# Performance work log

Hardware: AMD Instinct MI355X
Metric: run time of the kernel (lower is better)

Reference implementation:

```python
import jax, jax.numpy as jnp
import numpy as np
from jax import lax

M, T, WINDOW = 4096, 2048, 25
NEG_DIAG = -1e10  # matches alphas.fill_diagonal_(-1e10)


def setup_inputs() -> dict:
    key = jax.random.key(0)
    k_ys, k_a, k_r, k_b0, k_b1 = jax.random.split(key, 5)
    ys = jax.random.uniform(k_ys, (M, T), dtype=jnp.float32) * 10.0  # case counts
    alphas = 0.01 * jax.random.normal(k_a, (M, M), dtype=jnp.float32)
    repro = 1.0 + 0.01 * jax.random.normal(k_r, (M, WINDOW), dtype=jnp.float32)  # init ones
    b0 = 0.1 * jax.random.normal(k_b0, (M, 1), dtype=jnp.float32)
    b1 = 0.01 * jax.random.normal(k_b1, (M, 1), dtype=jnp.float32)
    t = jnp.arange(T, dtype=jnp.int32) + 1
    return {"ys": ys, "alphas": alphas, "repro": repro, "b0": b0, "b1": b1, "t": t}


def reference(ys, alphas, repro, b0, b1, t):
    m, _ = ys.shape
    window = repro.shape[1]
    offset = window - 1
    # metapopulation weights: sigmoid adjacency with diagonal forced to ~0
    diag = jnp.eye(m, dtype=bool)
    W = jax.nn.sigmoid(jnp.where(diag, jnp.asarray(NEG_DIAG, ys.dtype), alphas))
    # depthwise conv1d (cross-correlation), groups=M, VALID padding -> (M, T-window+1)
    Z = lax.conv_general_dilated(
        ys[None],                 # (1, M, T)
        repro[:, None, :],        # (M, 1, window)
        window_strides=(1,),
        padding='VALID',
        feature_group_count=m,
        dimension_numbers=('NCH', 'OIH', 'NCH'),
    )[0]                          # (M, T')
    ys_n = ys[:, offset:]         # (M, T')
    # beta_net: per-node softplus-linear in time -> (M, T), then narrow
    tt = t.astype(ys.dtype)
    beta = jax.nn.softplus(b0 + b1 * tt[None, :])[:, offset:]  # (M, T')
    return beta * (jax.nn.softplus(Z) + W @ ys_n)
```

## Files before the change

### kernel.cpp

```cpp
#include <hip/hip_runtime.h>
#include <stdint.h>

#define M_DIM 4096
#define T_DIM 2048
#define N_OUT 2024
#define N_PAD 2048
#define WIN   25
#define K_DIM 4096

typedef short bf16x8 __attribute__((ext_vector_type(8)));
typedef float f32x4  __attribute__((ext_vector_type(4)));

__device__ __forceinline__ unsigned short f2bf(float x) {
  unsigned u = __float_as_uint(x);
  u += 0x7FFF + ((u >> 16) & 1);
  return (unsigned short)(u >> 16);
}
__device__ __forceinline__ float bf2f(unsigned short h) {
  return __uint_as_float(((unsigned)h) << 16);
}

__device__ __forceinline__ void gl2lds16(const void* g, void* l) {
  __builtin_amdgcn_global_load_lds(
      (const __attribute__((address_space(1))) unsigned int*)g,
      (__attribute__((address_space(3))) unsigned int*)l, 16, 0, 0);
}

__global__ __launch_bounds__(256) void k_wcast(const float* __restrict__ alphas,
                                               unsigned short* __restrict__ Wb) {
  size_t i4 = ((size_t)blockIdx.x * 256 + threadIdx.x) * 4;
  const float4 v = *(const float4*)(alphas + i4);
  int row = (int)(i4 >> 12);
  int col = (int)(i4 & 4095);
  float a[4] = {v.x, v.y, v.z, v.w};
  ushort4 o;
  unsigned short* op = (unsigned short*)&o;
#pragma unroll
  for (int j = 0; j < 4; ++j) {
    float w = (row == col + j) ? 0.f : 1.f / (1.f + __expf(-a[j]));
    op[j] = f2bf(w);
  }
  *(ushort4*)(Wb + i4) = o;
}

__global__ __launch_bounds__(256) void k_conv(const float* __restrict__ ys,
                                              const float* __restrict__ repro,
                                              unsigned short* __restrict__ Sbf) {
  __shared__ float sy[256 + WIN - 1];
  __shared__ float sr[WIN];
  int m = blockIdx.y;
  int j0 = blockIdx.x * 256;
  int tid = threadIdx.x;
  sy[tid] = ys[(size_t)m * T_DIM + j0 + tid];
  if (tid < WIN - 1) {
    int jj = j0 + 256 + tid;
    sy[256 + tid] = (jj < T_DIM) ? ys[(size_t)m * T_DIM + jj] : 0.f;
  }
  if (tid < WIN) sr[tid] = repro[m * WIN + tid];
  __syncthreads();
  int j = j0 + tid;
  float z = 0.f;
#pragma unroll
  for (int k = 0; k < WIN; ++k) z += sy[tid + k] * sr[k];
  float sp = fmaxf(z, 0.f) + log1pf(__expf(-fabsf(z)));
  Sbf[(size_t)m * N_PAD + j] = (j < N_OUT) ? f2bf(sp) : (unsigned short)0;
}

__global__ __launch_bounds__(256) void k_transpose(const float* __restrict__ ys,
                                                   unsigned short* __restrict__ BT) {
  __shared__ float t[32][33];
  int n0 = blockIdx.x * 32;
  int k0 = blockIdx.y * 32;
  int tx = threadIdx.x;
  int ty = threadIdx.y;
#pragma unroll
  for (int r = 0; r < 4; ++r) {
    int kk = k0 + ty + r * 8;
    int n = n0 + tx;
    t[ty + r * 8][tx] = (n < N_OUT) ? ys[(size_t)kk * T_DIM + n + (WIN - 1)] : 0.f;
  }
  __syncthreads();
#pragma unroll
  for (int r = 0; r < 4; ++r) {
    int n = n0 + ty + r * 8;
    int kk = k0 + tx;
    BT[(size_t)n * K_DIM + kk] = f2bf(t[tx][ty + r * 8]);
  }
}

__global__ __launch_bounds__(256) void k_gemm(const unsigned short* __restrict__ Wb,
                                              const unsigned short* __restrict__ BT,
                                              const unsigned short* __restrict__ Sbf,
                                              const float* __restrict__ b0,
                                              const float* __restrict__ b1,
                                              float* __restrict__ out) {
  __shared__ __align__(16) unsigned short lA[128 * 32];
  __shared__ __align__(16) unsigned short lB[128 * 32];
  const int tid  = threadIdx.x;
  const int wave = tid >> 6;
  const int lane = tid & 63;
  const int wm = wave >> 1, wn = wave & 1;
  const int m16  = lane & 15;
  const int quad = lane >> 4;
  const int kof  = quad * 8;
  const int tileM = blockIdx.y * 128;
  const int tileN = blockIdx.x * 128;

  f32x4 acc[4][4];
#pragma unroll
  for (int i = 0; i < 4; ++i)
#pragma unroll
    for (int j = 0; j < 4; ++j) acc[i][j] = f32x4{0.f, 0.f, 0.f, 0.f};

  for (int kt = 0; kt < K_DIM / 32; ++kt) {
    const int k0 = kt * 32;
#pragma unroll
    for (int c = 0; c < 2; ++c) {
      int f = c * 256 + tid;
      int row = f >> 2;
      int colb = (f & 3) << 4;
      const char* gA = (const char*)Wb + (((size_t)(tileM + row) * K_DIM + k0) << 1) + colb;
      const char* gB = (const char*)BT + (((size_t)(tileN + row) * K_DIM + k0) << 1) + colb;
      gl2lds16(gA, (char*)lA + c * 4096 + wave * 1024);
      gl2lds16(gB, (char*)lB + c * 4096 + wave * 1024);
    }
    __syncthreads();
    bf16x8 aF[4], bF[4];
#pragma unroll
    for (int i = 0; i < 4; ++i) {
      aF[i] = *(const bf16x8*)&lA[(wm * 64 + i * 16 + m16) * 32 + kof];
      bF[i] = *(const bf16x8*)&lB[(wn * 64 + i * 16 + m16) * 32 + kof];
    }
#pragma unroll
    for (int i = 0; i < 4; ++i)
#pragma unroll
      for (int j = 0; j < 4; ++j)
        acc[i][j] = __builtin_amdgcn_mfma_f32_16x16x32_bf16(aF[i], bF[j], acc[i][j], 0, 0, 0);
    __syncthreads();
  }

#pragma unroll
  for (int j = 0; j < 4; ++j) {
    int gn = tileN + wn * 64 + j * 16 + m16;
    if (gn >= N_OUT) continue;
    float tval = (float)(gn + WIN);
#pragma unroll
    for (int i = 0; i < 4; ++i) {
#pragma unroll
      for (int r = 0; r < 4; ++r) {
        int gm = tileM + wm * 64 + i * 16 + quad * 4 + r;
        float x = b0[gm] + b1[gm] * tval;
        float beta = fmaxf(x, 0.f) + log1pf(__expf(-fabsf(x)));
        float s = bf2f(Sbf[(size_t)gm * N_PAD + gn]);
        out[(size_t)gm * N_OUT + gn] = beta * (s + acc[i][j][r]);
      }
    }
  }
}

extern "C" void kernel_launch(void* const* d_in, const int* in_sizes, int n_in,
                              void* d_out, int out_size, void* d_ws, size_t ws_size,
                              hipStream_t stream) {
  const float* ys     = (const float*)d_in[0];
  const float* alphas = (const float*)d_in[1];
  const float* repro  = (const float*)d_in[2];
  const float* b0     = (const float*)d_in[3];
  const float* b1     = (const float*)d_in[4];
  float* out = (float*)d_out;

  char* ws = (char*)d_ws;
  unsigned short* Wb  = (unsigned short*)ws;
  unsigned short* BT  = (unsigned short*)(ws + (size_t)M_DIM * K_DIM * 2);
  unsigned short* Sbf = (unsigned short*)(ws + (size_t)M_DIM * K_DIM * 2
                                             + (size_t)N_PAD * K_DIM * 2);

  k_wcast<<<(M_DIM * (size_t)K_DIM) / 4 / 256, 256, 0, stream>>>(alphas, Wb);
  k_conv<<<dim3(T_DIM / 256, M_DIM), 256, 0, stream>>>(ys, repro, Sbf);
  k_transpose<<<dim3(N_PAD / 32, K_DIM / 32), dim3(32, 8), 0, stream>>>(ys, BT);
  k_gemm<<<dim3(N_PAD / 128, M_DIM / 128), 256, 0, stream>>>(Wb, BT, Sbf, b0, b1, out);
}
```

Measured before the change: 295.3 us.

## Use 8 waves per GEMM block and widen sigmoid-cast stores

The GEMM block grows from 4 to 8 waves arranged 2x4, so each wave computes a 64x32 sub-tile with half as many accumulators. Each thread now issues one global-to-LDS load per operand per k-step, and the base pointers are hoisted out of the loop. This is meant to raise wave-level parallelism and hide memory latency, at the cost of more LDS fragment reads per MFMA and more barrier participants. Separately, the weight-cast kernel processes 8 elements per thread with 16-byte stores.

```diff
diff --git a/kernel.cpp b/kernel.cpp
--- a/kernel.cpp
+++ b/kernel.cpp
@@ -28,19 +28,20 @@
 
 __global__ __launch_bounds__(256) void k_wcast(const float* __restrict__ alphas,
                                                unsigned short* __restrict__ Wb) {
-  size_t i4 = ((size_t)blockIdx.x * 256 + threadIdx.x) * 4;
-  const float4 v = *(const float4*)(alphas + i4);
-  int row = (int)(i4 >> 12);
-  int col = (int)(i4 & 4095);
-  float a[4] = {v.x, v.y, v.z, v.w};
-  ushort4 o;
-  unsigned short* op = (unsigned short*)&o;
+  size_t i8 = ((size_t)blockIdx.x * 256 + threadIdx.x) * 8;
+  const float4 v0 = *(const float4*)(alphas + i8);
+  const float4 v1 = *(const float4*)(alphas + i8 + 4);
+  int row = (int)(i8 >> 12);
+  int col = (int)(i8 & 4095);
+  float a[8] = {v0.x, v0.y, v0.z, v0.w, v1.x, v1.y, v1.z, v1.w};
+  ushort4 o[2];
+  unsigned short* op = (unsigned short*)o;
 #pragma unroll
-  for (int j = 0; j < 4; ++j) {
+  for (int j = 0; j < 8; ++j) {
     float w = (row == col + j) ? 0.f : 1.f / (1.f + __expf(-a[j]));
     op[j] = f2bf(w);
   }
-  *(ushort4*)(Wb + i4) = o;
+  *(uint4*)(Wb + i8) = *(uint4*)o;
 }
 
 __global__ __launch_bounds__(256) void k_conv(const float* __restrict__ ys,
@@ -88,60 +89,60 @@
   }
 }
 
-__global__ __launch_bounds__(256) void k_gemm(const unsigned short* __restrict__ Wb,
-                                              const unsigned short* __restrict__ BT,
-                                              const unsigned short* __restrict__ Sbf,
-                                              const float* __restrict__ b0,
-                                              const float* __restrict__ b1,
-                                              float* __restrict__ out) {
+__global__ __launch_bounds__(512, 4) void k_gemm(const unsigned short* __restrict__ Wb,
+                                                 const unsigned short* __restrict__ BT,
+                                                 const unsigned short* __restrict__ Sbf,
+                                                 const float* __restrict__ b0,
+                                                 const float* __restrict__ b1,
+                                                 float* __restrict__ out) {
   __shared__ __align__(16) unsigned short lA[128 * 32];
   __shared__ __align__(16) unsigned short lB[128 * 32];
   const int tid  = threadIdx.x;
   const int wave = tid >> 6;
   const int lane = tid & 63;
-  const int wm = wave >> 1, wn = wave & 1;
+  const int wm = wave >> 2;
+  const int wn = wave & 3;
   const int m16  = lane & 15;
   const int quad = lane >> 4;
   const int kof  = quad * 8;
   const int tileM = blockIdx.y * 128;
   const int tileN = blockIdx.x * 128;
 
-  f32x4 acc[4][4];
+  const int srow  = tid >> 2;
+  const int scolb = (tid & 3) << 4;
+
+  f32x4 acc[4][2];
 #pragma unroll
   for (int i = 0; i < 4; ++i)
 #pragma unroll
-    for (int j = 0; j < 4; ++j) acc[i][j] = f32x4{0.f, 0.f, 0.f, 0.f};
+    for (int j = 0; j < 2; ++j) acc[i][j] = f32x4{0.f, 0.f, 0.f, 0.f};
+
+  const char* gA0 = (const char*)Wb + (((size_t)(tileM + srow) * K_DIM) << 1) + scolb;
+  const char* gB0 = (const char*)BT + (((size_t)(tileN + srow) * K_DIM) << 1) + scolb;
 
   for (int kt = 0; kt < K_DIM / 32; ++kt) {
-    const int k0 = kt * 32;
+    const size_t kb = (size_t)kt * 64;
+    gl2lds16(gA0 + kb, (char*)lA + wave * 1024);
+    gl2lds16(gB0 + kb, (char*)lB + wave * 1024);
+    __syncthreads();
+    bf16x8 aF[4], bF[2];
 #pragma unroll
-    for (int c = 0; c < 2; ++c) {
-      int f = c * 256 + tid;
-      int row = f >> 2;
-      int colb = (f & 3) << 4;
-      const char* gA = (const char*)Wb + (((size_t)(tileM + row) * K_DIM + k0) << 1) + colb;
-      const char* gB = (const char*)BT + (((size_t)(tileN + row) * K_DIM + k0) << 1) + colb;
-      gl2lds16(gA, (char*)lA + c * 4096 + wave * 1024);
-      gl2lds16(gB, (char*)lB + c * 4096 + wave * 1024);
-    }
-    __syncthreads();
-    bf16x8 aF[4], bF[4];
+    for (int i = 0; i < 4; ++i)
+      aF[i] = *(const bf16x8*)&lA[(wm * 64 + i * 16 + m16) * 32 + kof];
 #pragma unroll
-    for (int i = 0; i < 4; ++i) {
-      aF[i] = *(const bf16x8*)&lA[(wm * 64 + i * 16 + m16) * 32 + kof];
-      bF[i] = *(const bf16x8*)&lB[(wn * 64 + i * 16 + m16) * 32 + kof];
-    }
+    for (int j = 0; j < 2; ++j)
+      bF[j] = *(const bf16x8*)&lB[(wn * 32 + j * 16 + m16) * 32 + kof];
 #pragma unroll
     for (int i = 0; i < 4; ++i)
 #pragma unroll
-      for (int j = 0; j < 4; ++j)
+      for (int j = 0; j < 2; ++j)
         acc[i][j] = __builtin_amdgcn_mfma_f32_16x16x32_bf16(aF[i], bF[j], acc[i][j], 0, 0, 0);
     __syncthreads();
   }
 
 #pragma unroll
-  for (int j = 0; j < 4; ++j) {
-    int gn = tileN + wn * 64 + j * 16 + m16;
+  for (int j = 0; j < 2; ++j) {
+    int gn = tileN + wn * 32 + j * 16 + m16;
     if (gn >= N_OUT) continue;
     float tval = (float)(gn + WIN);
 #pragma unroll
@@ -174,8 +175,8 @@
   unsigned short* Sbf = (unsigned short*)(ws + (size_t)M_DIM * K_DIM * 2
                                              + (size_t)N_PAD * K_DIM * 2);
 
-  k_wcast<<<(M_DIM * (size_t)K_DIM) / 4 / 256, 256, 0, stream>>>(alphas, Wb);
+  k_wcast<<<(M_DIM * (size_t)K_DIM) / 8 / 256, 256, 0, stream>>>(alphas, Wb);
   k_conv<<<dim3(T_DIM / 256, M_DIM), 256, 0, stream>>>(ys, repro, Sbf);
   k_transpose<<<dim3(N_PAD / 32, K_DIM / 32), dim3(32, 8), 0, stream>>>(ys, BT);
-  k_gemm<<<dim3(N_PAD / 128, M_DIM / 128), 256, 0, stream>>>(Wb, BT, Sbf, b0, b1, out);
+  k_gemm<<<dim3(N_PAD / 128, M_DIM / 128), 512, 0, stream>>>(Wb, BT, Sbf, b0, b1, out);
 }
```

New measurement: 294.9 us. About the same (-0.1%).
